# Kernel tuning notes

Measured on AMD Instinct MI355X. Metric: run time of the kernel, lower is better.

## Reference

```python
import jax, jax.numpy as jnp
import numpy as np

N_USERS = 200000
N_ITEMS = 100000
N_NODES = N_USERS + N_ITEMS
EMBED_DIM = 64
N_LAYERS = 3
N_EDGES = 5000000
BATCH = 4096


def setup_inputs() -> dict:
    key = jax.random.key(0)
    ks = jax.random.split(key, 8)
    # Xavier-uniform-ish init for embedding tables
    lim = float(np.sqrt(6.0 / (N_USERS + EMBED_DIM)))
    user_emb = jax.random.uniform(ks[0], (N_USERS, EMBED_DIM), jnp.float32, -lim, lim)
    lim_i = float(np.sqrt(6.0 / (N_ITEMS + EMBED_DIM)))
    item_emb = jax.random.uniform(ks[1], (N_ITEMS, EMBED_DIM), jnp.float32, -lim_i, lim_i)
    # sparse normalized adjacency in COO form (values ~ 1/sqrt(du*di), use small positives)
    adj_vals = jax.random.uniform(ks[2], (N_EDGES,), jnp.float32, 0.0, 0.1)
    adj_rows = jax.random.randint(ks[3], (N_EDGES,), 0, N_NODES, jnp.int32)
    adj_cols = jax.random.randint(ks[4], (N_EDGES,), 0, N_NODES, jnp.int32)
    users = jax.random.randint(ks[5], (BATCH,), 0, N_USERS, jnp.int32)
    pos_items = jax.random.randint(ks[6], (BATCH,), 0, N_ITEMS, jnp.int32)
    neg_items = jax.random.randint(ks[7], (BATCH,), 0, N_ITEMS, jnp.int32)
    return {
        "user_emb": user_emb, "item_emb": item_emb, "adj_vals": adj_vals,
        "adj_rows": adj_rows, "adj_cols": adj_cols,
        "users": users, "pos_items": pos_items, "neg_items": neg_items,
    }


def _spmm(adj_rows, adj_cols, adj_vals, x):
    # y = A @ x for sparse COO A: gather source rows, scale, scatter-add to dest rows
    msgs = adj_vals[:, None] * x[adj_cols]          # [n_edges, d]
    return jax.ops.segment_sum(msgs, adj_rows, num_segments=N_NODES)


def reference(user_emb, item_emb, adj_vals, adj_rows, adj_cols, users, pos_items, neg_items):
    # E^0 = concat(user, item); E^k = A @ E^{k-1}; final = mean over k=0..K
    E = jnp.concatenate([user_emb, item_emb], axis=0)   # [N_NODES, d]
    acc = E
    cur = E
    for _ in range(N_LAYERS):
        cur = _spmm(adj_rows, adj_cols, adj_vals, cur)
        acc = acc + cur
    E_final = acc / jnp.asarray(N_LAYERS + 1, E.dtype)
    e_u = E_final[users]                         # users index into user block
    e_pos = E_final[N_USERS + pos_items]         # items offset by n_users
    e_neg = E_final[N_USERS + neg_items]
    return jnp.stack([e_u, e_pos, e_neg], axis=0)  # [3, B, d]
```

## Files before the change

### kernel.cpp

```cpp
#include <hip/hip_runtime.h>
#include <hip/hip_fp16.h>
#include <stdint.h>

#define N_USERS   200000
#define N_ITEMS   100000
#define N_NODES   300000
#define EMBED_DIM 64
#define N_EDGES   5000000
#define BATCH     4096

#define ROWS_PER_BUCKET 512
#define PART_K 586
#define PART_B 1024
#define CHUNK  4884
#define PART_L (PART_K * PART_B)
#define SCAN_T 1024
#define SCAN_NB (PART_L / SCAN_T)

#define VAL_SCALE 81920.0f
#define VAL_INV   (1.0f / 81920.0f)
#define FIN_CAP   10240

#define EMB_SCALE 1024.0f
#define EMB_INV   (1.0f / 1024.0f)

typedef float f32x2 __attribute__((ext_vector_type(2)));

__device__ __forceinline__ int swz(int b)     { return ((b & 7) << 7) | (b >> 3); }

__global__ void part_count(const int* __restrict__ rows, int* __restrict__ hist) {
    __shared__ int h[PART_K];
    for (int i = threadIdx.x; i < PART_K; i += blockDim.x) h[i] = 0;
    __syncthreads();
    int beg = blockIdx.x * CHUNK;
    int end = min(beg + CHUNK, N_EDGES);
    for (int i = beg + (int)threadIdx.x * 4; i < end; i += blockDim.x * 4) {
        int4 r4 = *(const int4*)(rows + i);
        atomicAdd(&h[r4.x >> 9], 1);
        atomicAdd(&h[r4.y >> 9], 1);
        atomicAdd(&h[r4.z >> 9], 1);
        atomicAdd(&h[r4.w >> 9], 1);
    }
    __syncthreads();
    for (int i = threadIdx.x; i < PART_K; i += blockDim.x)
        hist[blockIdx.x * PART_K + i] = h[i];
}

__global__ void scan_partial(const int* __restrict__ hist,
                             int* __restrict__ local_scan,
                             int* __restrict__ block_sums) {
    __shared__ int sh[SCAN_T];
    int tid = threadIdx.x;
    int gid = blockIdx.x * SCAN_T + tid;
    int p = gid & (PART_B - 1);
    int k = gid >> 10;
    int b = ((p & 127) << 3) | (p >> 7);
    int v = hist[b * PART_K + k];
    sh[tid] = v;
    __syncthreads();
    for (int off = 1; off < SCAN_T; off <<= 1) {
        int t = (tid >= off) ? sh[tid - off] : 0;
        __syncthreads();
        sh[tid] += t;
        __syncthreads();
    }
    local_scan[gid] = sh[tid] - v;
    if (tid == SCAN_T - 1) block_sums[blockIdx.x] = sh[tid];
}

__global__ void scan_addoff(const int* __restrict__ local_scan,
                            const int* __restrict__ block_sums,
                            int* __restrict__ sofs,
                            int* __restrict__ row_ptr) {
    __shared__ int sh[1024];
    int tid = threadIdx.x;
    int v = (tid < SCAN_NB) ? block_sums[tid] : 0;
    sh[tid] = v;
    __syncthreads();
    for (int off = 1; off < 1024; off <<= 1) {
        int t = (tid >= off) ? sh[tid - off] : 0;
        __syncthreads();
        sh[tid] += t;
        __syncthreads();
    }
    int base = (blockIdx.x == 0) ? 0 : sh[blockIdx.x - 1];
    int gid = blockIdx.x * SCAN_T + tid;
    sofs[gid] = local_scan[gid] + base;
    if (gid == 0) row_ptr[N_NODES] = N_EDGES;
}

__global__ void part_scatter(const int* __restrict__ rows,
                             const int* __restrict__ cols,
                             const float* __restrict__ vals,
                             const int* __restrict__ hist,
                             const int* __restrict__ sofs,
                             unsigned int* __restrict__ ppay,
                             unsigned short* __restrict__ prloc) {
    __shared__ int lcnt[PART_K];
    __shared__ int lbase[PART_K];
    __shared__ int gbase[PART_K];
    __shared__ int sc[1024];
    __shared__ unsigned int   pay[CHUNK];
    __shared__ unsigned short rl[CHUNK];
    __shared__ unsigned short bk[CHUNK];
    int b = blockIdx.x;
    int tid = threadIdx.x;
    int myp = swz(b);
    for (int i = tid; i < PART_K; i += 1024) {
        lcnt[i] = hist[b * PART_K + i];
        gbase[i] = sofs[i * PART_B + myp];
    }
    __syncthreads();
    int beg = b * CHUNK;
    int end = min(beg + CHUNK, N_EDGES);
    int n = end - beg;
    int v = (tid < PART_K) ? lcnt[tid] : 0;
    sc[tid] = v;
    __syncthreads();
    for (int off = 1; off < 1024; off <<= 1) {
        int t = (tid >= off) ? sc[tid - off] : 0;
        __syncthreads();
        sc[tid] += t;
        __syncthreads();
    }
    if (tid < PART_K) {
        int excl = sc[tid] - v;
        lbase[tid] = excl;
        lcnt[tid] = excl;
    }
    __syncthreads();
    for (int i = beg + tid * 4; i < end; i += 4096) {
        int4 r4 = *(const int4*)(rows + i);
        int4 c4 = *(const int4*)(cols + i);
        float4 v4 = *(const float4*)(vals + i);
        int rr[4] = {r4.x, r4.y, r4.z, r4.w};
        int cc[4] = {c4.x, c4.y, c4.z, c4.w};
        float vv[4] = {v4.x, v4.y, v4.z, v4.w};
        #pragma unroll
        for (int j = 0; j < 4; ++j) {
            int r = rr[j];
            int k = r >> 9;
            int p = atomicAdd(&lcnt[k], 1);
            unsigned int q = (unsigned int)min(8191, (int)(vv[j] * VAL_SCALE + 0.5f));
            pay[p] = (unsigned int)cc[j] | (q << 19);
            rl[p] = (unsigned short)(r & 511);
            bk[p] = (unsigned short)k;
        }
    }
    __syncthreads();
    for (int i = tid; i < n; i += 1024) {
        int k = bk[i];
        int a = gbase[k] + (i - lbase[k]);
        ppay[a] = pay[i];
        prloc[a] = rl[i];
    }
}

__global__ void csr_finalize(const unsigned int* __restrict__ ppay,
                             const unsigned short* __restrict__ prloc,
                             const int* __restrict__ sofs,
                             int* __restrict__ row_ptr,
                             unsigned int* __restrict__ sorted) {
    __shared__ int cnt[ROWS_PER_BUCKET];
    __shared__ int cur[ROWS_PER_BUCKET];
    __shared__ int sc[ROWS_PER_BUCKET];
    __shared__ unsigned int obuf[FIN_CAP];
    int k = blockIdx.x;
    int tid = threadIdx.x;
    int seg_beg = sofs[k * PART_B];
    int seg_end = (k + 1 < PART_K) ? sofs[(k + 1) * PART_B] : N_EDGES;
    int n = seg_end - seg_beg;

    cnt[tid] = 0;
    __syncthreads();
    for (int i = seg_beg + tid; i < seg_end; i += ROWS_PER_BUCKET)
        atomicAdd(&cnt[prloc[i]], 1);
    __syncthreads();

    int v = cnt[tid];
    sc[tid] = v;
    __syncthreads();
    for (int off = 1; off < 512; off <<= 1) {
        int t = (tid >= off) ? sc[tid - off] : 0;
        __syncthreads();
        sc[tid] += t;
        __syncthreads();
    }
    int excl = sc[tid] - v;

    int row = k * ROWS_PER_BUCKET + tid;
    if (row < N_NODES) row_ptr[row] = seg_beg + excl;
    cur[tid] = excl;
    __syncthreads();

    if (n <= FIN_CAP) {
        for (int i = seg_beg + tid; i < seg_end; i += ROWS_PER_BUCKET) {
            int r = prloc[i];
            int lp = atomicAdd(&cur[r], 1);
            obuf[lp] = ppay[i];
        }
        __syncthreads();
        for (int i = tid; i < n; i += ROWS_PER_BUCKET)
            sorted[seg_beg + i] = obuf[i];
    } else {
        for (int i = seg_beg + tid; i < seg_end; i += ROWS_PER_BUCKET) {
            int r = prloc[i];
            int lp = atomicAdd(&cur[r], 1);
            sorted[seg_beg + lp] = ppay[i];
        }
    }
}

__global__ void convert_emb(const float* __restrict__ ue,
                            const float* __restrict__ ie,
                            uint2* __restrict__ xf8) {
    int t = blockIdx.x * blockDim.x + threadIdx.x;
    if (t >= N_NODES * 8) return;
    int flat = t * 8;
    int row = flat >> 6;
    int off = flat & 63;
    const float* src = (row < N_USERS) ? (ue + (size_t)row * 64 + off)
                                       : (ie + (size_t)(row - N_USERS) * 64 + off);
    float4 a = ((const float4*)src)[0];
    float4 b = ((const float4*)src)[1];
    int lo = __builtin_amdgcn_cvt_pk_fp8_f32(a.x * EMB_SCALE, a.y * EMB_SCALE, 0, 0);
    lo     = __builtin_amdgcn_cvt_pk_fp8_f32(a.z * EMB_SCALE, a.w * EMB_SCALE, lo, 1);
    int hi = __builtin_amdgcn_cvt_pk_fp8_f32(b.x * EMB_SCALE, b.y * EMB_SCALE, 0, 0);
    hi     = __builtin_amdgcn_cvt_pk_fp8_f32(b.z * EMB_SCALE, b.w * EMB_SCALE, hi, 1);
    xf8[t] = make_uint2((unsigned int)lo, (unsigned int)hi);
}

#define ACCF8A(vv, u, A) { \
    f32x2 g0_ = __builtin_amdgcn_cvt_pk_f32_fp8((int)(u).x, 0); \
    f32x2 g1_ = __builtin_amdgcn_cvt_pk_f32_fp8((int)(u).x, 1); \
    f32x2 g2_ = __builtin_amdgcn_cvt_pk_f32_fp8((int)(u).y, 0); \
    f32x2 g3_ = __builtin_amdgcn_cvt_pk_f32_fp8((int)(u).y, 1); \
    A[0] += (vv) * g0_.x; A[1] += (vv) * g0_.y; \
    A[2] += (vv) * g1_.x; A[3] += (vv) * g1_.y; \
    A[4] += (vv) * g2_.x; A[5] += (vv) * g2_.y; \
    A[6] += (vv) * g3_.x; A[7] += (vv) * g3_.y; }

#define ACCHA(vv, r, A) { \
    const __half2* hp_ = (const __half2*)&(r); \
    float2 f0_ = __half22float2(hp_[0]); \
    float2 f1_ = __half22float2(hp_[1]); \
    float2 f2_ = __half22float2(hp_[2]); \
    float2 f3_ = __half22float2(hp_[3]); \
    A[0] += (vv) * f0_.x; A[1] += (vv) * f0_.y; \
    A[2] += (vv) * f1_.x; A[3] += (vv) * f1_.y; \
    A[4] += (vv) * f2_.x; A[5] += (vv) * f2_.y; \
    A[6] += (vv) * f3_.x; A[7] += (vv) * f3_.y; }

__global__ __launch_bounds__(256, 6)
void spmm_f8f8(const int* __restrict__ row_ptr,
               const unsigned int* __restrict__ sorted,
               const uint2* __restrict__ xf8,
               uint2* __restrict__ yf8) {
    int t = blockIdx.x * blockDim.x + threadIdx.x;
    int row = t >> 3;
    int l8 = t & 7;
    if (row >= N_NODES) return;
    int beg = row_ptr[row];
    int end = row_ptr[row + 1];
    float acc[8] = {0.f, 0.f, 0.f, 0.f, 0.f, 0.f, 0.f, 0.f};
    int e = beg;
    for (; e + 8 <= end; e += 8) {
        unsigned int cv[8];
        #pragma unroll
        for (int j = 0; j < 8; ++j) cv[j] = sorted[e + j];
        uint2 r[8];
        #pragma unroll
        for (int j = 0; j < 8; ++j)
            r[j] = xf8[(size_t)(cv[j] & 0x7FFFF) * 8 + l8];
        #pragma unroll
        for (int j = 0; j < 8; ++j) {
            float v = (float)(cv[j] >> 19) * VAL_INV;
            ACCF8A(v, r[j], acc);
        }
    }
    for (; e + 4 <= end; e += 4) {
        unsigned int cv[4];
        #pragma unroll
        for (int j = 0; j < 4; ++j) cv[j] = sorted[e + j];
        uint2 r[4];
        #pragma unroll
        for (int j = 0; j < 4; ++j)
            r[j] = xf8[(size_t)(cv[j] & 0x7FFFF) * 8 + l8];
        #pragma unroll
        for (int j = 0; j < 4; ++j) {
            float v = (float)(cv[j] >> 19) * VAL_INV;
            ACCF8A(v, r[j], acc);
        }
    }
    for (; e < end; ++e) {
        unsigned int cv = sorted[e];
        uint2 r0 = xf8[(size_t)(cv & 0x7FFFF) * 8 + l8];
        float v = (float)(cv >> 19) * VAL_INV;
        ACCF8A(v, r0, acc);
    }
    int lo = __builtin_amdgcn_cvt_pk_fp8_f32(acc[0], acc[1], 0, 0);
    lo     = __builtin_amdgcn_cvt_pk_fp8_f32(acc[2], acc[3], lo, 1);
    int hi = __builtin_amdgcn_cvt_pk_fp8_f32(acc[4], acc[5], 0, 0);
    hi     = __builtin_amdgcn_cvt_pk_fp8_f32(acc[6], acc[7], hi, 1);
    yf8[(size_t)row * 8 + l8] = make_uint2((unsigned int)lo, (unsigned int)hi);
}

__global__ __launch_bounds__(256, 6)
void spmm_f8f16(const int* __restrict__ row_ptr,
                const unsigned int* __restrict__ sorted,
                const uint2* __restrict__ xf8,
                __half* __restrict__ yh) {
    int t = blockIdx.x * blockDim.x + threadIdx.x;
    int row = t >> 3;
    int l8 = t & 7;
    if (row >= N_NODES) return;
    int beg = row_ptr[row];
    int end = row_ptr[row + 1];
    float acc[8] = {0.f, 0.f, 0.f, 0.f, 0.f, 0.f, 0.f, 0.f};
    int e = beg;
    for (; e + 8 <= end; e += 8) {
        unsigned int cv[8];
        #pragma unroll
        for (int j = 0; j < 8; ++j) cv[j] = sorted[e + j];
        uint2 r[8];
        #pragma unroll
        for (int j = 0; j < 8; ++j)
            r[j] = xf8[(size_t)(cv[j] & 0x7FFFF) * 8 + l8];
        #pragma unroll
        for (int j = 0; j < 8; ++j) {
            float v = (float)(cv[j] >> 19) * VAL_INV;
            ACCF8A(v, r[j], acc);
        }
    }
    for (; e + 4 <= end; e += 4) {
        unsigned int cv[4];
        #pragma unroll
        for (int j = 0; j < 4; ++j) cv[j] = sorted[e + j];
        uint2 r[4];
        #pragma unroll
        for (int j = 0; j < 4; ++j)
            r[j] = xf8[(size_t)(cv[j] & 0x7FFFF) * 8 + l8];
        #pragma unroll
        for (int j = 0; j < 4; ++j) {
            float v = (float)(cv[j] >> 19) * VAL_INV;
            ACCF8A(v, r[j], acc);
        }
    }
    for (; e < end; ++e) {
        unsigned int cv = sorted[e];
        uint2 r0 = xf8[(size_t)(cv & 0x7FFFF) * 8 + l8];
        float v = (float)(cv >> 19) * VAL_INV;
        ACCF8A(v, r0, acc);
    }
    float4 ov;
    ((__half2*)&ov)[0] = __floats2half2_rn(acc[0], acc[1]);
    ((__half2*)&ov)[1] = __floats2half2_rn(acc[2], acc[3]);
    ((__half2*)&ov)[2] = __floats2half2_rn(acc[4], acc[5]);
    ((__half2*)&ov)[3] = __floats2half2_rn(acc[6], acc[7]);
    ((float4*)yh)[(size_t)row * 8 + l8] = ov;
}

__global__ __launch_bounds__(256, 4)
void final_kernel(const int* __restrict__ row_ptr,
                  const unsigned int* __restrict__ sorted,
                  const float* __restrict__ user_emb,
                  const float* __restrict__ item_emb,
                  const uint2* __restrict__ x0f8,
                  const __half* __restrict__ E2h,
                  const int* __restrict__ users,
                  const int* __restrict__ pos_items,
                  const int* __restrict__ neg_items,
                  float* __restrict__ out) {
    int t = blockIdx.x * blockDim.x + threadIdx.x;
    int slot = t >> 4;
    int sub  = (t >> 3) & 1;
    int l8   = t & 7;
    if (slot >= 3 * BATCH) return;
    int which = slot >> 12;
    int idx   = slot & (BATCH - 1);
    int node;
    if (which == 0)      node = users[idx];
    else if (which == 1) node = N_USERS + pos_items[idx];
    else                 node = N_USERS + neg_items[idx];

    const float4* e2v = (const float4*)E2h;

    float a1[8] = {0.f, 0.f, 0.f, 0.f, 0.f, 0.f, 0.f, 0.f};
    float a3[8] = {0.f, 0.f, 0.f, 0.f, 0.f, 0.f, 0.f, 0.f};
    int beg = row_ptr[node];
    int end = row_ptr[node + 1];
    int nq = (end - beg) >> 2;
    for (int q = sub; q < nq; q += 2) {
        int e = beg + (q << 2);
        unsigned int cv[4];
        #pragma unroll
        for (int j = 0; j < 4; ++j) cv[j] = sorted[e + j];
        uint2 rx[4];
        float4 r2[4];
        #pragma unroll
        for (int j = 0; j < 4; ++j) {
            size_t col = (size_t)(cv[j] & 0x7FFFF);
            rx[j] = x0f8[col * 8 + l8];
            r2[j] = e2v[col * 8 + l8];
        }
        #pragma unroll
        for (int j = 0; j < 4; ++j) {
            float v = (float)(cv[j] >> 19) * VAL_INV;
            ACCF8A(v, rx[j], a1);
            ACCHA(v, r2[j], a3);
        }
    }
    if (sub == 0) {
        for (int e = beg + (nq << 2); e < end; ++e) {
            unsigned int cv = sorted[e];
            size_t col = (size_t)(cv & 0x7FFFF);
            uint2 rx = x0f8[col * 8 + l8];
            float4 r2 = e2v[col * 8 + l8];
            float v = (float)(cv >> 19) * VAL_INV;
            ACCF8A(v, rx, a1);
            ACCHA(v, r2, a3);
        }
    }
    #pragma unroll
    for (int i = 0; i < 8; ++i) {
        a1[i] += __shfl_xor(a1[i], 8);
        a3[i] += __shfl_xor(a3[i], 8);
    }
    if (sub) return;

    const float* t0 = (node < N_USERS) ? (user_emb + (size_t)node * 64)
                                       : (item_emb + (size_t)(node - N_USERS) * 64);
    float4 e0a = ((const float4*)t0)[l8 * 2];
    float4 e0b = ((const float4*)t0)[l8 * 2 + 1];

    float4 e2c = e2v[(size_t)node * 8 + l8];
    const __half2* h2 = (const __half2*)&e2c;
    float e2[8];
    {
        float2 b0 = __half22float2(h2[0]), b1 = __half22float2(h2[1]);
        float2 b2 = __half22float2(h2[2]), b3 = __half22float2(h2[3]);
        e2[0]=b0.x; e2[1]=b0.y; e2[2]=b1.x; e2[3]=b1.y;
        e2[4]=b2.x; e2[5]=b2.y; e2[6]=b3.x; e2[7]=b3.y;
    }
    float4 ra, rb;
    ra.x = (e0a.x + (a1[0] + e2[0] + a3[0]) * EMB_INV) * 0.25f;
    ra.y = (e0a.y + (a1[1] + e2[1] + a3[1]) * EMB_INV) * 0.25f;
    ra.z = (e0a.z + (a1[2] + e2[2] + a3[2]) * EMB_INV) * 0.25f;
    ra.w = (e0a.w + (a1[3] + e2[3] + a3[3]) * EMB_INV) * 0.25f;
    rb.x = (e0b.x + (a1[4] + e2[4] + a3[4]) * EMB_INV) * 0.25f;
    rb.y = (e0b.y + (a1[5] + e2[5] + a3[5]) * EMB_INV) * 0.25f;
    rb.z = (e0b.z + (a1[6] + e2[6] + a3[6]) * EMB_INV) * 0.25f;
    rb.w = (e0b.w + (a1[7] + e2[7] + a3[7]) * EMB_INV) * 0.25f;
    ((float4*)out)[(size_t)slot * 16 + l8 * 2]     = ra;
    ((float4*)out)[(size_t)slot * 16 + l8 * 2 + 1] = rb;
}

extern "C" void kernel_launch(void* const* d_in, const int* in_sizes, int n_in,
                              void* d_out, int out_size, void* d_ws, size_t ws_size,
                              hipStream_t stream) {
    const float* user_emb  = (const float*)d_in[0];
    const float* item_emb  = (const float*)d_in[1];
    const float* adj_vals  = (const float*)d_in[2];
    const int*   adj_rows  = (const int*)d_in[3];
    const int*   adj_cols  = (const int*)d_in[4];
    const int*   users     = (const int*)d_in[5];
    const int*   pos_items = (const int*)d_in[6];
    const int*   neg_items = (const int*)d_in[7];
    float* out = (float*)d_out;

    char* ws = (char*)d_ws;
    size_t off = 0;
    auto alloc = [&](size_t bytes) -> void* {
        void* p = ws + off;
        off = (off + bytes + 255) & ~(size_t)255;
        return p;
    };
    int*  hist       = (int*) alloc((size_t)(PART_L + 32) * sizeof(int));
    int*  local_scan = (int*) alloc((size_t)(PART_L + 32) * sizeof(int));
    int*  sofs       = (int*) alloc((size_t)(PART_L + 32) * sizeof(int));
    int*  block_sums = (int*) alloc((size_t)(SCAN_NB + 32) * sizeof(int));
    int*  row_ptr    = (int*) alloc((size_t)(N_NODES + 32) * sizeof(int));
    unsigned int*   ppay  = (unsigned int*)  alloc((size_t)N_EDGES * sizeof(unsigned int));
    unsigned short* prloc = (unsigned short*)alloc((size_t)N_EDGES * sizeof(unsigned short));
    unsigned int* sorted = (unsigned int*)alloc((size_t)N_EDGES * sizeof(unsigned int));
    uint2*  x0f8 = (uint2*) alloc((size_t)N_NODES * EMBED_DIM);
    uint2*  E1f8 = (uint2*) alloc((size_t)N_NODES * EMBED_DIM);
    __half* E2h  = (__half*)alloc((size_t)N_NODES * EMBED_DIM * sizeof(__half));

    const int TB = 256;

    part_count<<<PART_B, 1024, 0, stream>>>(adj_rows, hist);
    scan_partial<<<SCAN_NB, SCAN_T, 0, stream>>>(hist, local_scan, block_sums);
    scan_addoff<<<SCAN_NB, SCAN_T, 0, stream>>>(local_scan, block_sums, sofs, row_ptr);
    part_scatter<<<PART_B, 1024, 0, stream>>>(adj_rows, adj_cols, adj_vals, hist, sofs, ppay, prloc);
    csr_finalize<<<PART_K, ROWS_PER_BUCKET, 0, stream>>>(ppay, prloc, sofs, row_ptr, sorted);

    convert_emb<<<(N_NODES * 8 + TB - 1) / TB, TB, 0, stream>>>(user_emb, item_emb, x0f8);

    int spmm_blocks = (N_NODES * 8 + TB - 1) / TB;
    spmm_f8f8 <<<spmm_blocks, TB, 0, stream>>>(row_ptr, sorted, x0f8, E1f8);
    spmm_f8f16<<<spmm_blocks, TB, 0, stream>>>(row_ptr, sorted, E1f8, E2h);

    int final_blocks = (3 * BATCH * 16 + TB - 1) / TB;
    final_kernel<<<final_blocks, TB, 0, stream>>>(
        row_ptr, sorted, user_emb, item_emb, x0f8, E2h, users, pos_items, neg_items, out);
}
```

Baseline: 393.8 us.

## Fuse histogram with embedding conversion, use decoupled-lookback scan and wave-shuffle scans

Merges the partition-count kernel and the fp8 embedding conversion into one launch that also resets the lookback state. The two-kernel global scan becomes a single-pass decoupled-lookback scan that takes block order from a ticket counter. The shared-memory Hillis-Steele scans in the scatter and finalize kernels become wavefront shuffle scans with far fewer barriers. The goal is fewer launches and less sync overhead in CSR construction, at the cost of spin-waiting on global atomics, which depends on forward progress between blocks.

New measurement: 532.3 us. 35.2% more time.

```diff
diff --git a/kernel.cpp b/kernel.cpp
--- a/kernel.cpp
+++ b/kernel.cpp
@@ -21,6 +21,8 @@
 #define VAL_INV   (1.0f / 81920.0f)
 #define FIN_CAP   10240
 
+#define CONV_BLOCKS ((N_NODES * 8 + 1023) / 1024)
+
 #define EMB_SCALE 1024.0f
 #define EMB_INV   (1.0f / 1024.0f)
 
@@ -28,78 +30,157 @@
 
 __device__ __forceinline__ int swz(int b)     { return ((b & 7) << 7) | (b >> 3); }
 
-__global__ void part_count(const int* __restrict__ rows, int* __restrict__ hist) {
-    __shared__ int h[PART_K];
-    for (int i = threadIdx.x; i < PART_K; i += blockDim.x) h[i] = 0;
-    __syncthreads();
-    int beg = blockIdx.x * CHUNK;
-    int end = min(beg + CHUNK, N_EDGES);
-    for (int i = beg + (int)threadIdx.x * 4; i < end; i += blockDim.x * 4) {
-        int4 r4 = *(const int4*)(rows + i);
-        atomicAdd(&h[r4.x >> 9], 1);
-        atomicAdd(&h[r4.y >> 9], 1);
-        atomicAdd(&h[r4.z >> 9], 1);
-        atomicAdd(&h[r4.w >> 9], 1);
-    }
-    __syncthreads();
-    for (int i = threadIdx.x; i < PART_K; i += blockDim.x)
-        hist[blockIdx.x * PART_K + i] = h[i];
-}
-
-__global__ void scan_partial(const int* __restrict__ hist,
-                             int* __restrict__ local_scan,
-                             int* __restrict__ block_sums) {
-    __shared__ int sh[SCAN_T];
+__device__ __forceinline__ int wscan_incl(int x) {
+    #pragma unroll
+    for (int d = 1; d < 64; d <<= 1) {
+        int t = __shfl_up(x, d);
+        if ((int)(threadIdx.x & 63) >= d) x += t;
+    }
+    return x;
+}
+
+__device__ __forceinline__ int bscan1024(int v, int* ws) {
+    int tid = threadIdx.x, lane = tid & 63, wv = tid >> 6;
+    int x = wscan_incl(v);
+    if (lane == 63) ws[wv] = x;
+    __syncthreads();
+    if (tid < 16) {
+        int s = ws[tid];
+        #pragma unroll
+        for (int d = 1; d < 16; d <<= 1) {
+            int t = __shfl_up(s, d, 16);
+            if (tid >= d) s += t;
+        }
+        ws[tid] = s;
+    }
+    __syncthreads();
+    return x + (wv ? ws[wv - 1] : 0);
+}
+
+__device__ __forceinline__ int bscan512(int v, int* ws) {
+    int tid = threadIdx.x, lane = tid & 63, wv = tid >> 6;
+    int x = wscan_incl(v);
+    if (lane == 63) ws[wv] = x;
+    __syncthreads();
+    if (tid < 8) {
+        int s = ws[tid];
+        #pragma unroll
+        for (int d = 1; d < 8; d <<= 1) {
+            int t = __shfl_up(s, d, 8);
+            if (tid >= d) s += t;
+        }
+        ws[tid] = s;
+    }
+    __syncthreads();
+    return x + (wv ? ws[wv - 1] : 0);
+}
+
+__global__ __launch_bounds__(1024)
+void pc_conv(const int* __restrict__ rows, int* __restrict__ hist,
+             const float* __restrict__ ue, const float* __restrict__ ie,
+             uint2* __restrict__ xf8,
+             unsigned long long* __restrict__ lb_state, int* __restrict__ ticket) {
+    int bx = blockIdx.x;
     int tid = threadIdx.x;
-    int gid = blockIdx.x * SCAN_T + tid;
-    int p = gid & (PART_B - 1);
-    int k = gid >> 10;
+    if (bx < PART_B) {
+        __shared__ int h[PART_K];
+        for (int i = tid; i < PART_K; i += 1024) h[i] = 0;
+        __syncthreads();
+        int beg = bx * CHUNK;
+        int end = min(beg + CHUNK, N_EDGES);
+        for (int i = beg + tid * 4; i < end; i += 4096) {
+            int4 r4 = *(const int4*)(rows + i);
+            atomicAdd(&h[r4.x >> 9], 1);
+            atomicAdd(&h[r4.y >> 9], 1);
+            atomicAdd(&h[r4.z >> 9], 1);
+            atomicAdd(&h[r4.w >> 9], 1);
+        }
+        __syncthreads();
+        for (int i = tid; i < PART_K; i += 1024)
+            hist[bx * PART_K + i] = h[i];
+        return;
+    }
+    if (bx < PART_B + CONV_BLOCKS) {
+        int t = (bx - PART_B) * 1024 + tid;
+        if (t >= N_NODES * 8) return;
+        int flat = t * 8;
+        int row = flat >> 6;
+        int off = flat & 63;
+        const float* src = (row < N_USERS) ? (ue + (size_t)row * 64 + off)
+                                           : (ie + (size_t)(row - N_USERS) * 64 + off);
+        float4 a = ((const float4*)src)[0];
+        float4 b = ((const float4*)src)[1];
+        int lo = __builtin_amdgcn_cvt_pk_fp8_f32(a.x * EMB_SCALE, a.y * EMB_SCALE, 0, 0);
+        lo     = __builtin_amdgcn_cvt_pk_fp8_f32(a.z * EMB_SCALE, a.w * EMB_SCALE, lo, 1);
+        int hi = __builtin_amdgcn_cvt_pk_fp8_f32(b.x * EMB_SCALE, b.y * EMB_SCALE, 0, 0);
+        hi     = __builtin_amdgcn_cvt_pk_fp8_f32(b.z * EMB_SCALE, b.w * EMB_SCALE, hi, 1);
+        xf8[t] = make_uint2((unsigned int)lo, (unsigned int)hi);
+        return;
+    }
+    for (int i = tid; i < SCAN_NB; i += 1024) lb_state[i] = 0ULL;
+    if (tid == 0) ticket[0] = 0;
+}
+
+__global__ __launch_bounds__(1024)
+void scan_lookback(const int* __restrict__ hist,
+                   unsigned long long* __restrict__ state,
+                   int* __restrict__ ticket,
+                   int* __restrict__ sofs,
+                   int* __restrict__ row_ptr) {
+    __shared__ int ws[16];
+    __shared__ int sh_bid;
+    __shared__ int sh_base;
+    int tid = threadIdx.x;
+    if (tid == 0) sh_bid = atomicAdd(ticket, 1);
+    __syncthreads();
+    int bid = sh_bid;
+    int p = tid;
     int b = ((p & 127) << 3) | (p >> 7);
-    int v = hist[b * PART_K + k];
-    sh[tid] = v;
-    __syncthreads();
-    for (int off = 1; off < SCAN_T; off <<= 1) {
-        int t = (tid >= off) ? sh[tid - off] : 0;
-        __syncthreads();
-        sh[tid] += t;
-        __syncthreads();
-    }
-    local_scan[gid] = sh[tid] - v;
-    if (tid == SCAN_T - 1) block_sums[blockIdx.x] = sh[tid];
-}
-
-__global__ void scan_addoff(const int* __restrict__ local_scan,
-                            const int* __restrict__ block_sums,
-                            int* __restrict__ sofs,
-                            int* __restrict__ row_ptr) {
-    __shared__ int sh[1024];
-    int tid = threadIdx.x;
-    int v = (tid < SCAN_NB) ? block_sums[tid] : 0;
-    sh[tid] = v;
-    __syncthreads();
-    for (int off = 1; off < 1024; off <<= 1) {
-        int t = (tid >= off) ? sh[tid - off] : 0;
-        __syncthreads();
-        sh[tid] += t;
-        __syncthreads();
-    }
-    int base = (blockIdx.x == 0) ? 0 : sh[blockIdx.x - 1];
-    int gid = blockIdx.x * SCAN_T + tid;
-    sofs[gid] = local_scan[gid] + base;
+    int v = hist[b * PART_K + bid];
+    int incl = bscan1024(v, ws);
+    int total = ws[15];
+    if (tid == 0) {
+        if (bid == 0) {
+            __hip_atomic_store(&state[0], (2ULL << 32) | (unsigned int)total,
+                               __ATOMIC_RELEASE, __HIP_MEMORY_SCOPE_AGENT);
+            sh_base = 0;
+        } else {
+            __hip_atomic_store(&state[bid], (1ULL << 32) | (unsigned int)total,
+                               __ATOMIC_RELEASE, __HIP_MEMORY_SCOPE_AGENT);
+            unsigned int run = 0;
+            int j = bid - 1;
+            while (true) {
+                unsigned long long s = __hip_atomic_load(&state[j],
+                                        __ATOMIC_ACQUIRE, __HIP_MEMORY_SCOPE_AGENT);
+                unsigned int st = (unsigned int)(s >> 32);
+                if (st == 0) continue;
+                run += (unsigned int)s;
+                if (st == 2) break;
+                --j;
+            }
+            __hip_atomic_store(&state[bid], (2ULL << 32) | (unsigned int)(run + (unsigned int)total),
+                               __ATOMIC_RELEASE, __HIP_MEMORY_SCOPE_AGENT);
+            sh_base = (int)run;
+        }
+    }
+    __syncthreads();
+    int gid = bid * SCAN_T + tid;
+    sofs[gid] = sh_base + incl - v;
     if (gid == 0) row_ptr[N_NODES] = N_EDGES;
 }
 
-__global__ void part_scatter(const int* __restrict__ rows,
-                             const int* __restrict__ cols,
-                             const float* __restrict__ vals,
-                             const int* __restrict__ hist,
-                             const int* __restrict__ sofs,
-                             unsigned int* __restrict__ ppay,
-                             unsigned short* __restrict__ prloc) {
+__global__ __launch_bounds__(1024)
+void part_scatter(const int* __restrict__ rows,
+                  const int* __restrict__ cols,
+                  const float* __restrict__ vals,
+                  const int* __restrict__ hist,
+                  const int* __restrict__ sofs,
+                  unsigned int* __restrict__ ppay,
+                  unsigned short* __restrict__ prloc) {
     __shared__ int lcnt[PART_K];
     __shared__ int lbase[PART_K];
     __shared__ int gbase[PART_K];
-    __shared__ int sc[1024];
+    __shared__ int ws[16];
     __shared__ unsigned int   pay[CHUNK];
     __shared__ unsigned short rl[CHUNK];
     __shared__ unsigned short bk[CHUNK];
@@ -115,16 +196,10 @@
     int end = min(beg + CHUNK, N_EDGES);
     int n = end - beg;
     int v = (tid < PART_K) ? lcnt[tid] : 0;
-    sc[tid] = v;
-    __syncthreads();
-    for (int off = 1; off < 1024; off <<= 1) {
-        int t = (tid >= off) ? sc[tid - off] : 0;
-        __syncthreads();
-        sc[tid] += t;
-        __syncthreads();
-    }
+    int incl = bscan1024(v, ws);
+    int excl = incl - v;
+    __syncthreads();
     if (tid < PART_K) {
-        int excl = sc[tid] - v;
         lbase[tid] = excl;
         lcnt[tid] = excl;
     }
@@ -140,11 +215,11 @@
         for (int j = 0; j < 4; ++j) {
             int r = rr[j];
             int k = r >> 9;
-            int p = atomicAdd(&lcnt[k], 1);
+            int pcur = atomicAdd(&lcnt[k], 1);
             unsigned int q = (unsigned int)min(8191, (int)(vv[j] * VAL_SCALE + 0.5f));
-            pay[p] = (unsigned int)cc[j] | (q << 19);
-            rl[p] = (unsigned short)(r & 511);
-            bk[p] = (unsigned short)k;
+            pay[pcur] = (unsigned int)cc[j] | (q << 19);
+            rl[pcur] = (unsigned short)(r & 511);
+            bk[pcur] = (unsigned short)k;
         }
     }
     __syncthreads();
@@ -156,14 +231,15 @@
     }
 }
 
-__global__ void csr_finalize(const unsigned int* __restrict__ ppay,
-                             const unsigned short* __restrict__ prloc,
-                             const int* __restrict__ sofs,
-                             int* __restrict__ row_ptr,
-                             unsigned int* __restrict__ sorted) {
+__global__ __launch_bounds__(512)
+void csr_finalize(const unsigned int* __restrict__ ppay,
+                  const unsigned short* __restrict__ prloc,
+                  const int* __restrict__ sofs,
+                  int* __restrict__ row_ptr,
+                  unsigned int* __restrict__ sorted) {
     __shared__ int cnt[ROWS_PER_BUCKET];
     __shared__ int cur[ROWS_PER_BUCKET];
-    __shared__ int sc[ROWS_PER_BUCKET];
+    __shared__ int ws[8];
     __shared__ unsigned int obuf[FIN_CAP];
     int k = blockIdx.x;
     int tid = threadIdx.x;
@@ -178,15 +254,8 @@
     __syncthreads();
 
     int v = cnt[tid];
-    sc[tid] = v;
-    __syncthreads();
-    for (int off = 1; off < 512; off <<= 1) {
-        int t = (tid >= off) ? sc[tid - off] : 0;
-        __syncthreads();
-        sc[tid] += t;
-        __syncthreads();
-    }
-    int excl = sc[tid] - v;
+    int incl = bscan512(v, ws);
+    int excl = incl - v;
 
     int row = k * ROWS_PER_BUCKET + tid;
     if (row < N_NODES) row_ptr[row] = seg_beg + excl;
@@ -209,25 +278,6 @@
             sorted[seg_beg + lp] = ppay[i];
         }
     }
-}
-
-__global__ void convert_emb(const float* __restrict__ ue,
-                            const float* __restrict__ ie,
-                            uint2* __restrict__ xf8) {
-    int t = blockIdx.x * blockDim.x + threadIdx.x;
-    if (t >= N_NODES * 8) return;
-    int flat = t * 8;
-    int row = flat >> 6;
-    int off = flat & 63;
-    const float* src = (row < N_USERS) ? (ue + (size_t)row * 64 + off)
-                                       : (ie + (size_t)(row - N_USERS) * 64 + off);
-    float4 a = ((const float4*)src)[0];
-    float4 b = ((const float4*)src)[1];
-    int lo = __builtin_amdgcn_cvt_pk_fp8_f32(a.x * EMB_SCALE, a.y * EMB_SCALE, 0, 0);
-    lo     = __builtin_amdgcn_cvt_pk_fp8_f32(a.z * EMB_SCALE, a.w * EMB_SCALE, lo, 1);
-    int hi = __builtin_amdgcn_cvt_pk_fp8_f32(b.x * EMB_SCALE, b.y * EMB_SCALE, 0, 0);
-    hi     = __builtin_amdgcn_cvt_pk_fp8_f32(b.z * EMB_SCALE, b.w * EMB_SCALE, hi, 1);
-    xf8[t] = make_uint2((unsigned int)lo, (unsigned int)hi);
 }
 
 #define ACCF8A(vv, u, A) { \
@@ -475,11 +525,11 @@
         off = (off + bytes + 255) & ~(size_t)255;
         return p;
     };
-    int*  hist       = (int*) alloc((size_t)(PART_L + 32) * sizeof(int));
-    int*  local_scan = (int*) alloc((size_t)(PART_L + 32) * sizeof(int));
-    int*  sofs       = (int*) alloc((size_t)(PART_L + 32) * sizeof(int));
-    int*  block_sums = (int*) alloc((size_t)(SCAN_NB + 32) * sizeof(int));
-    int*  row_ptr    = (int*) alloc((size_t)(N_NODES + 32) * sizeof(int));
+    int*  hist    = (int*) alloc((size_t)(PART_L + 32) * sizeof(int));
+    int*  sofs    = (int*) alloc((size_t)(PART_L + 32) * sizeof(int));
+    int*  row_ptr = (int*) alloc((size_t)(N_NODES + 32) * sizeof(int));
+    unsigned long long* lb_state = (unsigned long long*)alloc((size_t)(SCAN_NB + 32) * sizeof(unsigned long long));
+    int*  ticket  = (int*) alloc(256);
     unsigned int*   ppay  = (unsigned int*)  alloc((size_t)N_EDGES * sizeof(unsigned int));
     unsigned short* prloc = (unsigned short*)alloc((size_t)N_EDGES * sizeof(unsigned short));
     unsigned int* sorted = (unsigned int*)alloc((size_t)N_EDGES * sizeof(unsigned int));
@@ -489,18 +539,14 @@
 
     const int TB = 256;
 
-    part_count<<<PART_B, 1024, 0, stream>>>(adj_rows, hist);
-    scan_partial<<<SCAN_NB, SCAN_T, 0, stream>>>(hist, local_scan, block_sums);
-    scan_addoff<<<SCAN_NB, SCAN_T, 0, stream>>>(local_scan, block_sums, sofs, row_ptr);
+    pc_conv<<<PART_B + CONV_BLOCKS + 1, 1024, 0, stream>>>(
+        adj_rows, hist, user_emb, item_emb, x0f8, lb_state, ticket);
+    scan_lookback<<<SCAN_NB, SCAN_T, 0, stream>>>(hist, lb_state, ticket, sofs, row_ptr);
     part_scatter<<<PART_B, 1024, 0, stream>>>(adj_rows, adj_cols, adj_vals, hist, sofs, ppay, prloc);
     csr_finalize<<<PART_K, ROWS_PER_BUCKET, 0, stream>>>(ppay, prloc, sofs, row_ptr, sorted);
-
-    convert_emb<<<(N_NODES * 8 + TB - 1) / TB, TB, 0, stream>>>(user_emb, item_emb, x0f8);
-
     int spmm_blocks = (N_NODES * 8 + TB - 1) / TB;
     spmm_f8f8 <<<spmm_blocks, TB, 0, stream>>>(row_ptr, sorted, x0f8, E1f8);
     spmm_f8f16<<<spmm_blocks, TB, 0, stream>>>(row_ptr, sorted, E1f8, E2h);
-
     int final_blocks = (3 * BATCH * 16 + TB - 1) / TB;
     final_kernel<<<final_blocks, TB, 0, stream>>>(
         row_ptr, sorted, user_emb, item_emb, x0f8, E2h, users, pos_items, neg_items, out);
```
